# Kernel optimization log

Hardware: AMD Instinct MI355X
Metric: run time of the kernel (lower is better)

## Reference

```python
import jax, jax.numpy as jnp
import numpy as np

HIDDEN = 768
HEADS = 12
HEAD_DIM = 64
SEQ = 512
DS_K = 64  # downsampling_k
EPS = 1e-6


def setup_inputs() -> dict:
    key = jax.random.key(0)
    ks = jax.random.split(key, 16)
    B = 32
    sd = 1.0 / DS_K
    glorot = jax.nn.initializers.lecun_normal()  # flax default_kernel_init
    inp = {
        "query": jax.random.normal(ks[0], (B, SEQ, HIDDEN), jnp.float32),
        "key": jax.random.normal(ks[1], (B, SEQ, HIDDEN), jnp.float32),
        "value": jax.random.normal(ks[2], (B, SEQ, HIDDEN), jnp.float32),
        "step": 0,
        # learned Linformer-style downsampling projections [k, s]
        "W_kds": sd * jax.random.normal(ks[3], (DS_K, SEQ), jnp.float32),
        "W_vds": sd * jax.random.normal(ks[4], (DS_K, SEQ), jnp.float32),
        # DenseGeneral qkv kernels [d, n, h] and biases [n, h]
        "Wq": glorot(ks[5], (HIDDEN, HEADS, HEAD_DIM), jnp.float32),
        "bq": jnp.zeros((HEADS, HEAD_DIM), jnp.float32),
        "Wk": glorot(ks[6], (HIDDEN, HEADS, HEAD_DIM), jnp.float32),
        "bk": jnp.zeros((HEADS, HEAD_DIM), jnp.float32),
        "Wv": glorot(ks[7], (HIDDEN, HEADS, HEAD_DIM), jnp.float32),
        "bv": jnp.zeros((HEADS, HEAD_DIM), jnp.float32),
        # out projection contracts (n, h) -> hidden
        "Wout": glorot(ks[8], (HEADS * HEAD_DIM, HIDDEN), jnp.float32).reshape(HEADS, HEAD_DIM, HIDDEN),
        "bout": jnp.zeros((HIDDEN,), jnp.float32),
    }
    return inp


def reference(query, key, value, step, W_kds, W_vds, Wq, bq, Wk, bk, Wv, bv, Wout, bout):
    # Linformer-style downsample of keys/values along sequence: [b,s,d] -> [b,k,d]
    key_ds = jnp.einsum("ks,bsd->bkd", W_kds, key)
    val_ds = jnp.einsum("ks,bsd->bkd", W_vds, value)

    # per-head projections
    queries = jnp.einsum("bqd,dnh->bqnh", query, Wq) + bq    # [b,q,n,h]
    keys = jnp.einsum("bkd,dnh->bknh", key_ds, Wk) + bk      # [b,k,n,h]
    values = jnp.einsum("bkd,dnh->bknh", val_ds, Wv) + bv    # [b,k,n,h]

    # kernelized linear attention with elu feature map (mask=False path)
    phi_q = jax.nn.elu(queries) + 1.0
    phi_k = jax.nn.elu(keys) + 1.0
    s = jnp.einsum("bknd,bknh->bndh", phi_k, values)          # [b,n,h,h] KV state
    z = jnp.sum(phi_k, axis=1)                                 # [b,n,h]
    qs = jnp.einsum("bqnd,bndh->bqnh", phi_q, s)
    qz = jnp.einsum("bqnd,bnd->bqn", phi_q, z) + EPS
    a_v = qs / qz[..., None]                                   # [b,q,n,h]

    out = jnp.einsum("bqnh,nhD->bqD", a_v, Wout) + bout        # [b,q,hidden]
    return out
```

## Files before the change

kernel.cpp:

```cpp
#include <hip/hip_runtime.h>

typedef unsigned short u16;
typedef u16 u16x8 __attribute__((ext_vector_type(8)));
typedef __bf16 bf16;
typedef bf16 bf16x8 __attribute__((ext_vector_type(8)));
typedef float f32x4 __attribute__((ext_vector_type(4)));

__device__ __forceinline__ float bf2f(u16 v) {
  union { unsigned u; float f; } x; x.u = ((unsigned)v) << 16; return x.f;
}
__device__ __forceinline__ u16 f2bf(float f) {
  union { float f; unsigned u; } x; x.f = f;
  unsigned u = x.u;
  u += 0x7fffu + ((u >> 16) & 1u);
  return (u16)(u >> 16);
}

#define GLDS16(g, l) __builtin_amdgcn_global_load_lds( \
    (const __attribute__((address_space(1))) unsigned int*)(const void*)(g), \
    (__attribute__((address_space(3))) unsigned int*)(void*)(l), 16, 0, 0)

__global__ __launch_bounds__(256) void convert_k(
    const float* __restrict__ wk, const float* __restrict__ wv,
    const float* __restrict__ b0, const float* __restrict__ b1,
    const float* __restrict__ b2, const float* __restrict__ b3,
    u16* __restrict__ dstW, u16* __restrict__ dstB) {
  const int i = blockIdx.x * 256 + threadIdx.x;
  if (i < 32768)      dstW[i] = f2bf(wk[i]);
  else if (i < 65536) dstW[i] = f2bf(wv[i - 32768]);
  else {
    int j = i - 65536, s = j / 768, si = j % 768;
    const float* src = (s == 0) ? b0 : (s == 1) ? b1 : (s == 2) ? b2 : b3;
    dstB[j] = f2bf(src[si]);
  }
}

__global__ __launch_bounds__(256) void f32_to_bf16_k(
    const float* __restrict__ in, u16* __restrict__ out) {
  const int i = blockIdx.x * 256 + threadIdx.x;
  f32x4 a = *(const f32x4*)&in[(size_t)i * 8];
  f32x4 b = *(const f32x4*)&in[(size_t)i * 8 + 4];
  u16x8 w;
  #pragma unroll
  for (int j = 0; j < 4; ++j) { w[j] = f2bf(a[j]); w[4 + j] = f2bf(b[j]); }
  *(u16x8*)&out[(size_t)i * 8] = w;
}

__global__ __launch_bounds__(256) void transpose4_k(
    const float* __restrict__ w0, const float* __restrict__ w1,
    const float* __restrict__ w2, const float* __restrict__ w3,
    u16* __restrict__ out) {
  const float* W = (blockIdx.z == 0) ? w0 : (blockIdx.z == 1) ? w1 : (blockIdx.z == 2) ? w2 : w3;
  u16* O = out + (size_t)blockIdx.z * 768 * 768;
  __shared__ u16 T[64][72];
  const int t = threadIdx.x;
  const int r0 = blockIdx.x * 64, c0 = blockIdx.y * 64;
  #pragma unroll
  for (int p = 0; p < 2; ++p) {
    int v = t + p * 256;
    int r = v / 8, c = (v % 8) * 8;
    f32x4 x0 = *(const f32x4*)&W[(size_t)(r0 + r) * 768 + c0 + c];
    f32x4 x1 = *(const f32x4*)&W[(size_t)(r0 + r) * 768 + c0 + c + 4];
    #pragma unroll
    for (int i = 0; i < 4; ++i) { T[r][c + i] = f2bf(x0[i]); T[r][c + 4 + i] = f2bf(x1[i]); }
  }
  __syncthreads();
  #pragma unroll
  for (int p = 0; p < 2; ++p) {
    int v = t + p * 256;
    int r = v / 8, c = (v % 8) * 8;
    u16x8 tv;
    #pragma unroll
    for (int i = 0; i < 8; ++i) tv[i] = T[c + i][r];
    *(u16x8*)&O[(size_t)(c0 + r) * 768 + r0 + c] = tv;
  }
}

template<int ACT, bool OF32>
__global__ __launch_bounds__(256) void gemm97_k(
    const u16* __restrict__ A, int lda,
    const u16* __restrict__ Bt, int ldb,
    void* __restrict__ Craw, int ldc,
    const u16* __restrict__ bias, int K)
{
  __shared__ u16 As[128 * 32];
  __shared__ u16 Bs[128 * 32];
  const int mt = blockIdx.x * 128, nt = blockIdx.y * 128;
  const int t = threadIdx.x, wave = t >> 6, lane = t & 63;
  const int wm = (wave >> 1) * 64, wn = (wave & 1) * 64;
  const int lrow = lane & 15, quad = lane >> 4;
  f32x4 acc[4][4] = {};

  for (int k0 = 0; k0 < K; k0 += 32) {
    __syncthreads();
    #pragma unroll
    for (int p = 0; p < 2; ++p) {
      const int s = wave * 128 + p * 64 + lane;
      const int r = s >> 2, c = (s & 3) * 8;
      const int lb = (wave * 128 + p * 64) * 8;
      GLDS16(&A[(size_t)(mt + r) * lda + k0 + c], &As[lb]);
      GLDS16(&Bt[(size_t)(nt + r) * ldb + k0 + c], &Bs[lb]);
    }
    __syncthreads();

    bf16x8 av[4], bv[4];
    #pragma unroll
    for (int i = 0; i < 4; ++i) av[i] = *(const bf16x8*)&As[(wm + i * 16 + lrow) * 32 + quad * 8];
    #pragma unroll
    for (int j = 0; j < 4; ++j) bv[j] = *(const bf16x8*)&Bs[(wn + j * 16 + lrow) * 32 + quad * 8];
    #pragma unroll
    for (int i = 0; i < 4; ++i)
      #pragma unroll
      for (int j = 0; j < 4; ++j)
        acc[i][j] = __builtin_amdgcn_mfma_f32_16x16x32_bf16(av[i], bv[j], acc[i][j], 0, 0, 0);
  }

  #pragma unroll
  for (int i = 0; i < 4; ++i) {
    #pragma unroll
    for (int j = 0; j < 4; ++j) {
      const int col = nt + wn + j * 16 + lrow;
      const float badd = bias ? bf2f(bias[col]) : 0.0f;
      #pragma unroll
      for (int r = 0; r < 4; ++r) {
        const int row = mt + wm + i * 16 + quad * 4 + r;
        float v = acc[i][j][r] + badd;
        if constexpr (ACT == 1) v = v > 0.0f ? v + 1.0f : __expf(v);
        if constexpr (OF32) ((float*)Craw)[(size_t)row * ldc + col] = v;
        else                ((u16*)Craw)[(size_t)row * ldc + col] = f2bf(v);
      }
    }
  }
}

template<int BM, int BN, int BK, int WM, int WN, bool NN, int ACT,
         bool AF32, bool BF32, bool OF32>
__global__ __launch_bounds__(256) void gemm_k(
    const void* __restrict__ Araw, int lda,
    const void* __restrict__ Braw, int ldb,
    void* __restrict__ Craw, int ldc,
    const u16* __restrict__ bias,
    int K, int nDiv,
    long long offA_b, long long offA_n,
    long long offB_b, long long offB_n,
    long long offC_b, long long offC_n,
    long long offBias_b)
{
  constexpr int LDSK = BK + 8;
  __shared__ u16 As[BM][LDSK];
  __shared__ u16 Bs[BN][LDSK];

  const int z  = blockIdx.z;
  const int bb = z / nDiv, ni = z % nDiv;
  const long long dA = bb * offA_b + ni * offA_n;
  const long long dB = bb * offB_b + ni * offB_n;
  const long long dC = bb * offC_b + ni * offC_n;
  const u16*   A16 = AF32 ? nullptr : ((const u16*)Araw) + dA;
  const float* A32 = AF32 ? ((const float*)Araw) + dA : nullptr;
  const u16*   B16 = BF32 ? nullptr : ((const u16*)Braw) + dB;
  const float* B32 = BF32 ? ((const float*)Braw) + dB : nullptr;
  u16*   C16 = OF32 ? nullptr : ((u16*)Craw) + dC;
  float* C32 = OF32 ? ((float*)Craw) + dC : nullptr;
  if (bias) bias += bb * offBias_b;

  const int mt = blockIdx.x * BM;
  const int nt = blockIdx.y * BN;
  const int t = threadIdx.x;
  const int wave = t >> 6, lane = t & 63;
  constexpr int WAVES_N = BN / WN;
  const int wm = (wave / WAVES_N) * WM;
  const int wn = (wave % WAVES_N) * WN;
  constexpr int FM = WM / 16, FN = WN / 16;
  const int lrow = lane & 15, quad = lane >> 4;

  f32x4 acc[FM][FN] = {};

  for (int k0 = 0; k0 < K; k0 += BK) {
    __syncthreads();
    #pragma unroll
    for (int p = 0; p < (BM * BK / 8) / 256; ++p) {
      int v = t + p * 256;
      int r = v / (BK / 8);
      int c = (v % (BK / 8)) * 8;
      size_t idx = (size_t)(mt + r) * lda + k0 + c;
      if constexpr (!AF32) {
        *(u16x8*)&As[r][c] = *(const u16x8*)&A16[idx];
      } else {
        f32x4 x0 = *(const f32x4*)&A32[idx];
        f32x4 x1 = *(const f32x4*)&A32[idx + 4];
        u16x8 w;
        #pragma unroll
        for (int i = 0; i < 4; ++i) { w[i] = f2bf(x0[i]); w[4 + i] = f2bf(x1[i]); }
        *(u16x8*)&As[r][c] = w;
      }
    }
    if constexpr (!NN) {
      #pragma unroll
      for (int p = 0; p < (BN * BK / 8) / 256; ++p) {
        int v = t + p * 256;
        int r = v / (BK / 8);
        int c = (v % (BK / 8)) * 8;
        size_t idx = (size_t)(nt + r) * ldb + k0 + c;
        if constexpr (!BF32) {
          *(u16x8*)&Bs[r][c] = *(const u16x8*)&B16[idx];
        } else {
          f32x4 x0 = *(const f32x4*)&B32[idx];
          f32x4 x1 = *(const f32x4*)&B32[idx + 4];
          u16x8 w;
          #pragma unroll
          for (int i = 0; i < 4; ++i) { w[i] = f2bf(x0[i]); w[4 + i] = f2bf(x1[i]); }
          *(u16x8*)&Bs[r][c] = w;
        }
      }
    } else {
      static_assert(!NN || (BN == 128 && BK == 32), "NN staging is fixed-shape");
      int n  = t & 127;
      int kh = (t >> 7) * 16;
      u16x8 t0, t1;
      if constexpr (!BF32) {
        #pragma unroll
        for (int i = 0; i < 8; ++i) t0[i] = B16[(size_t)(k0 + kh + i) * ldb + nt + n];
        #pragma unroll
        for (int i = 0; i < 8; ++i) t1[i] = B16[(size_t)(k0 + kh + 8 + i) * ldb + nt + n];
      } else {
        #pragma unroll
        for (int i = 0; i < 8; ++i) t0[i] = f2bf(B32[(size_t)(k0 + kh + i) * ldb + nt + n]);
        #pragma unroll
        for (int i = 0; i < 8; ++i) t1[i] = f2bf(B32[(size_t)(k0 + kh + 8 + i) * ldb + nt + n]);
      }
      *(u16x8*)&Bs[n][kh]     = t0;
      *(u16x8*)&Bs[n][kh + 8] = t1;
    }
    __syncthreads();

    bf16x8 av[FM], bv[FN];
    #pragma unroll
    for (int i = 0; i < FM; ++i) av[i] = *(const bf16x8*)&As[wm + i * 16 + lrow][quad * 8];
    #pragma unroll
    for (int j = 0; j < FN; ++j) bv[j] = *(const bf16x8*)&Bs[wn + j * 16 + lrow][quad * 8];
    #pragma unroll
    for (int i = 0; i < FM; ++i)
      #pragma unroll
      for (int j = 0; j < FN; ++j)
        acc[i][j] = __builtin_amdgcn_mfma_f32_16x16x32_bf16(av[i], bv[j], acc[i][j], 0, 0, 0);
  }

  #pragma unroll
  for (int i = 0; i < FM; ++i) {
    #pragma unroll
    for (int j = 0; j < FN; ++j) {
      const int col = nt + wn + j * 16 + lrow;
      float badd = bias ? bf2f(bias[col]) : 0.0f;
      #pragma unroll
      for (int r = 0; r < 4; ++r) {
        const int row = mt + wm + i * 16 + quad * 4 + r;
        float v = acc[i][j][r] + badd;
        if constexpr (ACT == 1) v = v > 0.0f ? v + 1.0f : __expf(v);
        if constexpr (ACT == 3) { if (bb == 0) v = v > 0.0f ? v + 1.0f : __expf(v); }
        if constexpr (OF32) C32[(size_t)row * ldc + col] = v;
        else                C16[(size_t)row * ldc + col] = f2bf(v);
      }
    }
  }
}

__global__ __launch_bounds__(256) void kv_state_k(
    const u16* __restrict__ phi_k, const u16* __restrict__ vals,
    u16* __restrict__ sT, float* __restrict__ z)
{
  __shared__ float pk[64][65];
  __shared__ float vv[64][65];
  const int x = blockIdx.x;
  const int b = x / 12, n = x % 12;
  const int t = threadIdx.x;
  const u16* pkg = phi_k + (size_t)b * 64 * 768 + n * 64;
  const u16* vvg = vals  + (size_t)b * 64 * 768 + n * 64;
  #pragma unroll
  for (int p = 0; p < 2; ++p) {
    int v = t + p * 256;
    int r = v / 8, c = (v % 8) * 8;
    u16x8 a  = *(const u16x8*)&pkg[(size_t)r * 768 + c];
    u16x8 bq = *(const u16x8*)&vvg[(size_t)r * 768 + c];
    #pragma unroll
    for (int i = 0; i < 8; ++i) { pk[r][c + i] = bf2f(a[i]); vv[r][c + i] = bf2f(bq[i]); }
  }
  __syncthreads();
  const int d0 = (t >> 4) * 4, h0 = (t & 15) * 4;
  float s4[4][4] = {};
  for (int k = 0; k < 64; ++k) {
    float pv[4], vb[4];
    #pragma unroll
    for (int i = 0; i < 4; ++i) { pv[i] = pk[k][d0 + i]; vb[i] = vv[k][h0 + i]; }
    #pragma unroll
    for (int i = 0; i < 4; ++i)
      #pragma unroll
      for (int j = 0; j < 4; ++j) s4[i][j] += pv[i] * vb[j];
  }
  const size_t base = (size_t)x * 4096;
  #pragma unroll
  for (int i = 0; i < 4; ++i)
    #pragma unroll
    for (int j = 0; j < 4; ++j)
      sT[base + (size_t)(h0 + j) * 64 + d0 + i] = f2bf(s4[i][j]);
  if (t < 64) {
    float zz = 0.f;
    for (int k = 0; k < 64; ++k) zz += pk[k][t];
    z[(size_t)x * 64 + t] = zz;
  }
}

__global__ __launch_bounds__(256) void attn_av_k(
    u16* __restrict__ phi_q,
    const u16* __restrict__ sT,
    const float* __restrict__ zbuf)
{
  __shared__ u16 As[64 * 72];
  __shared__ u16 Bs[64 * 72];
  __shared__ float zv[64];
  __shared__ float zpart[4][64];
  __shared__ float zq[64];
  const int x = blockIdx.x, y = blockIdx.y;
  const int b = y / 12, n = y % 12;
  const int t = threadIdx.x;
  u16* Abase = phi_q + (size_t)b * 512 * 768 + (size_t)x * 64 * 768 + n * 64;
  const u16* Bbase = sT + (size_t)y * 4096;
  if (t < 64) zv[t] = zbuf[(size_t)y * 64 + t];
  #pragma unroll
  for (int p = 0; p < 2; ++p) {
    int v = t + p * 256;
    int r = v >> 3, c = (v & 7) * 8;
    *(u16x8*)&As[r * 72 + c] = *(const u16x8*)&Abase[(size_t)r * 768 + c];
    *(u16x8*)&Bs[r * 72 + c] = *(const u16x8*)&Bbase[r * 64 + c];
  }
  __syncthreads();
  {
    int r = t & 63, seg = t >> 6;
    float s = 0.f;
    #pragma unroll
    for (int j = 0; j < 16; ++j) s += bf2f(As[r * 72 + seg * 16 + j]) * zv[seg * 16 + j];
    zpart[seg][r] = s;
  }
  __syncthreads();
  if (t < 64) {
    float s = zpart[0][t] + zpart[1][t] + zpart[2][t] + zpart[3][t];
    zq[t] = 1.0f / (s + 1e-6f);
  }
  const int wave = t >> 6, lane = t & 63;
  const int wm = (wave >> 1) * 32, wn = (wave & 1) * 32;
  const int lrow = lane & 15, quad = lane >> 4;
  f32x4 acc[2][2] = {};
  #pragma unroll
  for (int c = 0; c < 2; ++c) {
    bf16x8 av[2], bv[2];
    #pragma unroll
    for (int i = 0; i < 2; ++i) av[i] = *(const bf16x8*)&As[(wm + i * 16 + lrow) * 72 + c * 32 + quad * 8];
    #pragma unroll
    for (int j = 0; j < 2; ++j) bv[j] = *(const bf16x8*)&Bs[(wn + j * 16 + lrow) * 72 + c * 32 + quad * 8];
    #pragma unroll
    for (int i = 0; i < 2; ++i)
      #pragma unroll
      for (int j = 0; j < 2; ++j)
        acc[i][j] = __builtin_amdgcn_mfma_f32_16x16x32_bf16(av[i], bv[j], acc[i][j], 0, 0, 0);
  }
  __syncthreads();
  #pragma unroll
  for (int i = 0; i < 2; ++i)
    #pragma unroll
    for (int j = 0; j < 2; ++j) {
      const int col = wn + j * 16 + lrow;
      #pragma unroll
      for (int r = 0; r < 4; ++r) {
        const int row = wm + i * 16 + quad * 4 + r;
        Abase[(size_t)row * 768 + col] = f2bf(acc[i][j][r] * zq[row]);
      }
    }
}

__global__ void tagfill_k(float* out, float val, int n) {
  int i = blockIdx.x * 256 + threadIdx.x;
  if (i < n) out[i] = val;
}

extern "C" void kernel_launch(void* const* d_in, const int* in_sizes, int n_in,
                              void* d_out, int out_size, void* d_ws, size_t ws_size,
                              hipStream_t stream) {
  (void)out_size;
  float* out = (float*)d_out;

  int o;
  if (n_in >= 14 && in_sizes[3] == 1) o = 4;
  else if (n_in == 13) o = 3;
  else { tagfill_k<<<4, 256, 0, stream>>>(out, 77.0f, 1024); return; }
  if (in_sizes[0] != 12582912 || in_sizes[o + 0] != 32768 || in_sizes[o + 2] != 589824) {
    tagfill_k<<<4, 256, 0, stream>>>(out, 88.0f, 1024); return;
  }

  const float* query = (const float*)d_in[0];
  const float* key   = (const float*)d_in[1];
  const float* value = (const float*)d_in[2];
  const float* W_kds = (const float*)d_in[o + 0];
  const float* W_vds = (const float*)d_in[o + 1];
  const float* Wq   = (const float*)d_in[o + 2];
  const float* bq   = (const float*)d_in[o + 3];
  const float* Wk   = (const float*)d_in[o + 4];
  const float* bk   = (const float*)d_in[o + 5];
  const float* Wv   = (const float*)d_in[o + 6];
  const float* bv   = (const float*)d_in[o + 7];
  const float* Wout = (const float*)d_in[o + 8];
  const float* bout = (const float*)d_in[o + 9];

  const size_t NEED_SMALL = 42604544;
  const size_t NEED_BIG   = 55187456;
  if (ws_size < NEED_SMALL) { tagfill_k<<<4, 256, 0, stream>>>(out, 123.0f, 1024); return; }
  const bool big = (ws_size >= NEED_BIG);

  char* base = (char*)d_ws;
  u16 *WT, *q_bf = nullptr, *key_ds, *val_ds, *phi_k, *vals, *phi_q, *sT, *Wds_c, *bias_c;
  float* zbuf;
  WT = (u16*)base;
  if (big) {
    char* B = base + 4718592;
    q_bf   = (u16*)B;
    key_ds = (u16*)B;
    val_ds = (u16*)(B + 3145728);
    phi_k  = (u16*)(B + 6291456);
    vals   = (u16*)(B + 9437184);
    sT     = (u16*)B;
    zbuf   = (float*)(B + 3145728);
    phi_q  = (u16*)(base + 29884416);
    Wds_c  = (u16*)(base + 55050240);
    bias_c = (u16*)(base + 55181312);
  } else {
    key_ds = (u16*)(base + 4718592);
    val_ds = (u16*)(base + 7864320);
    sT     = (u16*)(base + 4718592);
    zbuf   = (float*)(base + 7864320);
    phi_k  = (u16*)(base + 11010048);
    vals   = (u16*)(base + 14155776);
    phi_q  = (u16*)(base + 17301504);
    Wds_c  = (u16*)(base + 42467328);
    bias_c = (u16*)(base + 42598400);
  }
  u16* a_v = phi_q;
  u16* WqT   = WT;
  u16* WkT   = WT + 768 * 768;
  u16* WvT   = WT + 2 * 768 * 768;
  u16* WoutT = WT + 3 * 768 * 768;
  u16* Wkds_c = Wds_c;
  u16* Wvds_c = Wds_c + 32768;
  u16* bq_c = bias_c, *bk_c = bias_c + 768, *bv_c = bias_c + 1536, *bout_c = bias_c + 2304;

  convert_k<<<268, 256, 0, stream>>>(W_kds, W_vds, bq, bk, bv, bout, Wds_c, bias_c);
  transpose4_k<<<dim3(12, 12, 4), 256, 0, stream>>>(Wq, Wk, Wv, Wout, WT);

  if (big) {
    f32_to_bf16_k<<<6144, 256, 0, stream>>>(query, q_bf);
    gemm97_k<1, false><<<dim3(128, 6), 256, 0, stream>>>(
        q_bf, 768, WqT, 768, phi_q, 768, bq_c, 768);
  } else {
    gemm_k<128, 128, 32, 64, 64, false, 1, true, false, false><<<dim3(128, 6, 1), 256, 0, stream>>>(
        query, 768, WqT, 768, phi_q, 768, bq_c, 768, 1, 0, 0, 0, 0, 0, 0, 0);
  }

  gemm_k<64, 128, 32, 64, 32, true, 0, false, true, false><<<dim3(1, 6, 32), 256, 0, stream>>>(
      Wkds_c, 512, key, 768, key_ds, 768, nullptr, 512, 1,
      0, 0, (long long)512 * 768, 0, (long long)64 * 768, 0, 0);
  gemm_k<64, 128, 32, 64, 32, true, 0, false, true, false><<<dim3(1, 6, 32), 256, 0, stream>>>(
      Wvds_c, 512, value, 768, val_ds, 768, nullptr, 512, 1,
      0, 0, (long long)512 * 768, 0, (long long)64 * 768, 0, 0);

  gemm_k<64, 64, 32, 32, 32, false, 3, false, false, false><<<dim3(32, 12, 2), 256, 0, stream>>>(
      key_ds, 768, WkT, 768, phi_k, 768, bk_c, 768, 1,
      1572864, 0, 589824, 0, 1572864, 0, 768);

  kv_state_k<<<dim3(384), 256, 0, stream>>>(phi_k, vals, sT, zbuf);

  attn_av_k<<<dim3(8, 384), 256, 0, stream>>>(phi_q, sT, zbuf);

  gemm97_k<0, true><<<dim3(128, 6), 256, 0, stream>>>(
      a_v, 768, WoutT, 768, out, 768, bout_c, 768);
}
```

Measured before the change: 329.1 us.

## Merge prep kernels into one launch and fuse key/value downsampling GEMMs

Three preprocessing kernels (weight transpose, query bf16 conversion, small weight/bias conversion) are merged into one launch with block-range dispatch. The two separate key/value downsampling GEMMs become a single ds_k kernel covering both, with coalesced row-wise f32 loads that are converted and transposed into shared memory. The small-workspace fallback path is removed and the generic GEMM template is specialised. This cuts launch count and improves the strided B loads of the old NN staging, but the downsampling kernel runs only 384 blocks with a 64-row tile.

Measured after the change: 313.3 us. 1.05x faster.

```diff
diff --git a/kernel.cpp b/kernel.cpp
--- a/kernel.cpp
+++ b/kernel.cpp
@@ -20,60 +20,117 @@
     (const __attribute__((address_space(1))) unsigned int*)(const void*)(g), \
     (__attribute__((address_space(3))) unsigned int*)(void*)(l), 16, 0, 0)
 
-__global__ __launch_bounds__(256) void convert_k(
-    const float* __restrict__ wk, const float* __restrict__ wv,
+__global__ __launch_bounds__(256) void prep_k(
+    const float* __restrict__ Wq, const float* __restrict__ Wk,
+    const float* __restrict__ Wv, const float* __restrict__ Wout,
+    const float* __restrict__ query,
+    const float* __restrict__ wkds, const float* __restrict__ wvds,
     const float* __restrict__ b0, const float* __restrict__ b1,
     const float* __restrict__ b2, const float* __restrict__ b3,
-    u16* __restrict__ dstW, u16* __restrict__ dstB) {
-  const int i = blockIdx.x * 256 + threadIdx.x;
-  if (i < 32768)      dstW[i] = f2bf(wk[i]);
-  else if (i < 65536) dstW[i] = f2bf(wv[i - 32768]);
-  else {
-    int j = i - 65536, s = j / 768, si = j % 768;
-    const float* src = (s == 0) ? b0 : (s == 1) ? b1 : (s == 2) ? b2 : b3;
-    dstB[j] = f2bf(src[si]);
-  }
-}
-
-__global__ __launch_bounds__(256) void f32_to_bf16_k(
-    const float* __restrict__ in, u16* __restrict__ out) {
-  const int i = blockIdx.x * 256 + threadIdx.x;
-  f32x4 a = *(const f32x4*)&in[(size_t)i * 8];
-  f32x4 b = *(const f32x4*)&in[(size_t)i * 8 + 4];
-  u16x8 w;
-  #pragma unroll
-  for (int j = 0; j < 4; ++j) { w[j] = f2bf(a[j]); w[4 + j] = f2bf(b[j]); }
-  *(u16x8*)&out[(size_t)i * 8] = w;
-}
-
-__global__ __launch_bounds__(256) void transpose4_k(
-    const float* __restrict__ w0, const float* __restrict__ w1,
-    const float* __restrict__ w2, const float* __restrict__ w3,
-    u16* __restrict__ out) {
-  const float* W = (blockIdx.z == 0) ? w0 : (blockIdx.z == 1) ? w1 : (blockIdx.z == 2) ? w2 : w3;
-  u16* O = out + (size_t)blockIdx.z * 768 * 768;
+    u16* __restrict__ WT, u16* __restrict__ q_bf,
+    u16* __restrict__ dstW, u16* __restrict__ dstB)
+{
   __shared__ u16 T[64][72];
+  const int blk = blockIdx.x;
   const int t = threadIdx.x;
-  const int r0 = blockIdx.x * 64, c0 = blockIdx.y * 64;
-  #pragma unroll
-  for (int p = 0; p < 2; ++p) {
-    int v = t + p * 256;
-    int r = v / 8, c = (v % 8) * 8;
-    f32x4 x0 = *(const f32x4*)&W[(size_t)(r0 + r) * 768 + c0 + c];
-    f32x4 x1 = *(const f32x4*)&W[(size_t)(r0 + r) * 768 + c0 + c + 4];
-    #pragma unroll
-    for (int i = 0; i < 4; ++i) { T[r][c + i] = f2bf(x0[i]); T[r][c + 4 + i] = f2bf(x1[i]); }
-  }
-  __syncthreads();
-  #pragma unroll
-  for (int p = 0; p < 2; ++p) {
-    int v = t + p * 256;
-    int r = v / 8, c = (v % 8) * 8;
-    u16x8 tv;
-    #pragma unroll
-    for (int i = 0; i < 8; ++i) tv[i] = T[c + i][r];
-    *(u16x8*)&O[(size_t)(c0 + r) * 768 + r0 + c] = tv;
-  }
+  if (blk < 576) {
+    const int bz = blk / 144, rr = blk % 144;
+    const int r0 = (rr / 12) * 64, c0 = (rr % 12) * 64;
+    const float* W = (bz == 0) ? Wq : (bz == 1) ? Wk : (bz == 2) ? Wv : Wout;
+    u16* O = WT + (size_t)bz * 768 * 768;
+    #pragma unroll
+    for (int p = 0; p < 2; ++p) {
+      int v = t + p * 256;
+      int r = v / 8, c = (v % 8) * 8;
+      f32x4 x0 = *(const f32x4*)&W[(size_t)(r0 + r) * 768 + c0 + c];
+      f32x4 x1 = *(const f32x4*)&W[(size_t)(r0 + r) * 768 + c0 + c + 4];
+      #pragma unroll
+      for (int i = 0; i < 4; ++i) { T[r][c + i] = f2bf(x0[i]); T[r][c + 4 + i] = f2bf(x1[i]); }
+    }
+    __syncthreads();
+    #pragma unroll
+    for (int p = 0; p < 2; ++p) {
+      int v = t + p * 256;
+      int r = v / 8, c = (v % 8) * 8;
+      u16x8 tv;
+      #pragma unroll
+      for (int i = 0; i < 8; ++i) tv[i] = T[c + i][r];
+      *(u16x8*)&O[(size_t)(c0 + r) * 768 + r0 + c] = tv;
+    }
+  } else if (blk < 6720) {
+    const size_t i = (size_t)(blk - 576) * 256 + t;
+    f32x4 a = *(const f32x4*)&query[i * 8];
+    f32x4 b = *(const f32x4*)&query[i * 8 + 4];
+    u16x8 w;
+    #pragma unroll
+    for (int j = 0; j < 4; ++j) { w[j] = f2bf(a[j]); w[4 + j] = f2bf(b[j]); }
+    *(u16x8*)&q_bf[i * 8] = w;
+  } else {
+    const int i = (blk - 6720) * 256 + t;
+    if (i < 32768)      dstW[i] = f2bf(wkds[i]);
+    else if (i < 65536) dstW[i] = f2bf(wvds[i - 32768]);
+    else {
+      int j = i - 65536, s = j / 768, si = j % 768;
+      const float* src = (s == 0) ? b0 : (s == 1) ? b1 : (s == 2) ? b2 : b3;
+      dstB[j] = f2bf(src[si]);
+    }
+  }
+}
+
+__global__ __launch_bounds__(256) void ds_k(
+    const u16* __restrict__ Wds,
+    const float* __restrict__ key, const float* __restrict__ value,
+    u16* __restrict__ key_ds)
+{
+  __shared__ u16 As[64][40];
+  __shared__ u16 Bs[128][36];
+  const int pair = blockIdx.y >> 5, b = blockIdx.y & 31;
+  const float* src = (pair ? value : key) + (size_t)b * 512 * 768;
+  const u16* W = Wds + pair * 32768;
+  u16* dst = key_ds + (size_t)pair * 1572864 + (size_t)b * 49152;
+  const int nt = blockIdx.x * 128;
+  const int t = threadIdx.x, wave = t >> 6, lane = t & 63;
+  const int wm = (wave >> 1) * 32, wn = (wave & 1) * 64;
+  const int lrow = lane & 15, quad = lane >> 4;
+  const int kk = t >> 5, n4 = (t & 31) * 4;
+
+  f32x4 acc[2][4] = {};
+  for (int k0 = 0; k0 < 512; k0 += 32) {
+    __syncthreads();
+    {
+      int r = t >> 2, c = (t & 3) * 8;
+      *(u16x8*)&As[r][c] = *(const u16x8*)&W[(size_t)r * 512 + k0 + c];
+    }
+    #pragma unroll
+    for (int p = 0; p < 4; ++p) {
+      int k = kk + p * 8;
+      f32x4 x = *(const f32x4*)&src[(size_t)(k0 + k) * 768 + nt + n4];
+      #pragma unroll
+      for (int i = 0; i < 4; ++i) Bs[n4 + i][k] = f2bf(x[i]);
+    }
+    __syncthreads();
+    bf16x8 av[2], bv[4];
+    #pragma unroll
+    for (int i = 0; i < 2; ++i) av[i] = *(const bf16x8*)&As[wm + i * 16 + lrow][quad * 8];
+    #pragma unroll
+    for (int j = 0; j < 4; ++j) bv[j] = *(const bf16x8*)&Bs[wn + j * 16 + lrow][quad * 8];
+    #pragma unroll
+    for (int i = 0; i < 2; ++i)
+      #pragma unroll
+      for (int j = 0; j < 4; ++j)
+        acc[i][j] = __builtin_amdgcn_mfma_f32_16x16x32_bf16(av[i], bv[j], acc[i][j], 0, 0, 0);
+  }
+  #pragma unroll
+  for (int i = 0; i < 2; ++i)
+    #pragma unroll
+    for (int j = 0; j < 4; ++j) {
+      const int col = nt + wn + j * 16 + lrow;
+      #pragma unroll
+      for (int r = 0; r < 4; ++r) {
+        const int row = wm + i * 16 + quad * 4 + r;
+        dst[(size_t)row * 768 + col] = f2bf(acc[i][j][r]);
+      }
+    }
 }
 
 template<int ACT, bool OF32>
@@ -133,36 +190,20 @@
   }
 }
 
-template<int BM, int BN, int BK, int WM, int WN, bool NN, int ACT,
-         bool AF32, bool BF32, bool OF32>
-__global__ __launch_bounds__(256) void gemm_k(
-    const void* __restrict__ Araw, int lda,
-    const void* __restrict__ Braw, int ldb,
-    void* __restrict__ Craw, int ldc,
+template<int BM, int BN, int BK, int WM, int WN>
+__global__ __launch_bounds__(256) void gemmkv_k(
+    const u16* __restrict__ A, int lda,
+    const u16* __restrict__ B, int ldb,
+    u16* __restrict__ C, int ldc,
     const u16* __restrict__ bias,
-    int K, int nDiv,
-    long long offA_b, long long offA_n,
-    long long offB_b, long long offB_n,
-    long long offC_b, long long offC_n,
-    long long offBias_b)
+    int K,
+    long long offA_b, long long offB_b, long long offC_b, long long offBias_b)
 {
   constexpr int LDSK = BK + 8;
   __shared__ u16 As[BM][LDSK];
   __shared__ u16 Bs[BN][LDSK];
-
-  const int z  = blockIdx.z;
-  const int bb = z / nDiv, ni = z % nDiv;
-  const long long dA = bb * offA_b + ni * offA_n;
-  const long long dB = bb * offB_b + ni * offB_n;
-  const long long dC = bb * offC_b + ni * offC_n;
-  const u16*   A16 = AF32 ? nullptr : ((const u16*)Araw) + dA;
-  const float* A32 = AF32 ? ((const float*)Araw) + dA : nullptr;
-  const u16*   B16 = BF32 ? nullptr : ((const u16*)Braw) + dB;
-  const float* B32 = BF32 ? ((const float*)Braw) + dB : nullptr;
-  u16*   C16 = OF32 ? nullptr : ((u16*)Craw) + dC;
-  float* C32 = OF32 ? ((float*)Craw) + dC : nullptr;
-  if (bias) bias += bb * offBias_b;
-
+  const int bb = blockIdx.z;
+  A += bb * offA_b; B += bb * offB_b; C += bb * offC_b; bias += bb * offBias_b;
   const int mt = blockIdx.x * BM;
   const int nt = blockIdx.y * BN;
   const int t = threadIdx.x;
@@ -172,7 +213,6 @@
   const int wn = (wave % WAVES_N) * WN;
   constexpr int FM = WM / 16, FN = WN / 16;
   const int lrow = lane & 15, quad = lane >> 4;
-
   f32x4 acc[FM][FN] = {};
 
   for (int k0 = 0; k0 < K; k0 += BK) {
@@ -180,59 +220,16 @@
     #pragma unroll
     for (int p = 0; p < (BM * BK / 8) / 256; ++p) {
       int v = t + p * 256;
-      int r = v / (BK / 8);
-      int c = (v % (BK / 8)) * 8;
-      size_t idx = (size_t)(mt + r) * lda + k0 + c;
-      if constexpr (!AF32) {
-        *(u16x8*)&As[r][c] = *(const u16x8*)&A16[idx];
-      } else {
-        f32x4 x0 = *(const f32x4*)&A32[idx];
-        f32x4 x1 = *(const f32x4*)&A32[idx + 4];
-        u16x8 w;
-        #pragma unroll
-        for (int i = 0; i < 4; ++i) { w[i] = f2bf(x0[i]); w[4 + i] = f2bf(x1[i]); }
-        *(u16x8*)&As[r][c] = w;
-      }
-    }
-    if constexpr (!NN) {
-      #pragma unroll
-      for (int p = 0; p < (BN * BK / 8) / 256; ++p) {
-        int v = t + p * 256;
-        int r = v / (BK / 8);
-        int c = (v % (BK / 8)) * 8;
-        size_t idx = (size_t)(nt + r) * ldb + k0 + c;
-        if constexpr (!BF32) {
-          *(u16x8*)&Bs[r][c] = *(const u16x8*)&B16[idx];
-        } else {
-          f32x4 x0 = *(const f32x4*)&B32[idx];
-          f32x4 x1 = *(const f32x4*)&B32[idx + 4];
-          u16x8 w;
-          #pragma unroll
-          for (int i = 0; i < 4; ++i) { w[i] = f2bf(x0[i]); w[4 + i] = f2bf(x1[i]); }
-          *(u16x8*)&Bs[r][c] = w;
-        }
-      }
-    } else {
-      static_assert(!NN || (BN == 128 && BK == 32), "NN staging is fixed-shape");
-      int n  = t & 127;
-      int kh = (t >> 7) * 16;
-      u16x8 t0, t1;
-      if constexpr (!BF32) {
-        #pragma unroll
-        for (int i = 0; i < 8; ++i) t0[i] = B16[(size_t)(k0 + kh + i) * ldb + nt + n];
-        #pragma unroll
-        for (int i = 0; i < 8; ++i) t1[i] = B16[(size_t)(k0 + kh + 8 + i) * ldb + nt + n];
-      } else {
-        #pragma unroll
-        for (int i = 0; i < 8; ++i) t0[i] = f2bf(B32[(size_t)(k0 + kh + i) * ldb + nt + n]);
-        #pragma unroll
-        for (int i = 0; i < 8; ++i) t1[i] = f2bf(B32[(size_t)(k0 + kh + 8 + i) * ldb + nt + n]);
-      }
-      *(u16x8*)&Bs[n][kh]     = t0;
-      *(u16x8*)&Bs[n][kh + 8] = t1;
-    }
-    __syncthreads();
-
+      int r = v / (BK / 8), c = (v % (BK / 8)) * 8;
+      *(u16x8*)&As[r][c] = *(const u16x8*)&A[(size_t)(mt + r) * lda + k0 + c];
+    }
+    #pragma unroll
+    for (int p = 0; p < (BN * BK / 8) / 256; ++p) {
+      int v = t + p * 256;
+      int r = v / (BK / 8), c = (v % (BK / 8)) * 8;
+      *(u16x8*)&Bs[r][c] = *(const u16x8*)&B[(size_t)(nt + r) * ldb + k0 + c];
+    }
+    __syncthreads();
     bf16x8 av[FM], bv[FN];
     #pragma unroll
     for (int i = 0; i < FM; ++i) av[i] = *(const bf16x8*)&As[wm + i * 16 + lrow][quad * 8];
@@ -244,24 +241,20 @@
       for (int j = 0; j < FN; ++j)
         acc[i][j] = __builtin_amdgcn_mfma_f32_16x16x32_bf16(av[i], bv[j], acc[i][j], 0, 0, 0);
   }
-
-  #pragma unroll
-  for (int i = 0; i < FM; ++i) {
+  #pragma unroll
+  for (int i = 0; i < FM; ++i)
     #pragma unroll
     for (int j = 0; j < FN; ++j) {
       const int col = nt + wn + j * 16 + lrow;
-      float badd = bias ? bf2f(bias[col]) : 0.0f;
+      const float badd = bf2f(bias[col]);
       #pragma unroll
       for (int r = 0; r < 4; ++r) {
         const int row = mt + wm + i * 16 + quad * 4 + r;
         float v = acc[i][j][r] + badd;
-        if constexpr (ACT == 1) v = v > 0.0f ? v + 1.0f : __expf(v);
-        if constexpr (ACT == 3) { if (bb == 0) v = v > 0.0f ? v + 1.0f : __expf(v); }
-        if constexpr (OF32) C32[(size_t)row * ldc + col] = v;
-        else                C16[(size_t)row * ldc + col] = f2bf(v);
+        if (bb == 0) v = v > 0.0f ? v + 1.0f : __expf(v);
+        C[(size_t)row * ldc + col] = f2bf(v);
       }
     }
-  }
 }
 
 __global__ __launch_bounds__(256) void kv_state_k(
@@ -310,9 +303,7 @@
 }
 
 __global__ __launch_bounds__(256) void attn_av_k(
-    u16* __restrict__ phi_q,
-    const u16* __restrict__ sT,
-    const float* __restrict__ zbuf)
+    u16* __restrict__ phi_q, const u16* __restrict__ sT, const float* __restrict__ zbuf)
 {
   __shared__ u16 As[64 * 72];
   __shared__ u16 Bs[64 * 72];
@@ -409,69 +400,38 @@
   const float* Wout = (const float*)d_in[o + 8];
   const float* bout = (const float*)d_in[o + 9];
 
-  const size_t NEED_SMALL = 42604544;
-  const size_t NEED_BIG   = 55187456;
-  if (ws_size < NEED_SMALL) { tagfill_k<<<4, 256, 0, stream>>>(out, 123.0f, 1024); return; }
-  const bool big = (ws_size >= NEED_BIG);
+  const size_t NEED = 55187456;
+  if (ws_size < NEED) { tagfill_k<<<4, 256, 0, stream>>>(out, 123.0f, 1024); return; }
 
   char* base = (char*)d_ws;
-  u16 *WT, *q_bf = nullptr, *key_ds, *val_ds, *phi_k, *vals, *phi_q, *sT, *Wds_c, *bias_c;
-  float* zbuf;
-  WT = (u16*)base;
-  if (big) {
-    char* B = base + 4718592;
-    q_bf   = (u16*)B;
-    key_ds = (u16*)B;
-    val_ds = (u16*)(B + 3145728);
-    phi_k  = (u16*)(B + 6291456);
-    vals   = (u16*)(B + 9437184);
-    sT     = (u16*)B;
-    zbuf   = (float*)(B + 3145728);
-    phi_q  = (u16*)(base + 29884416);
-    Wds_c  = (u16*)(base + 55050240);
-    bias_c = (u16*)(base + 55181312);
-  } else {
-    key_ds = (u16*)(base + 4718592);
-    val_ds = (u16*)(base + 7864320);
-    sT     = (u16*)(base + 4718592);
-    zbuf   = (float*)(base + 7864320);
-    phi_k  = (u16*)(base + 11010048);
-    vals   = (u16*)(base + 14155776);
-    phi_q  = (u16*)(base + 17301504);
-    Wds_c  = (u16*)(base + 42467328);
-    bias_c = (u16*)(base + 42598400);
-  }
+  u16*   WT     = (u16*)base;
+  char*  Breg   = base + 4718592;
+  u16*   q_bf   = (u16*)Breg;
+  u16*   key_ds = (u16*)Breg;
+  u16*   sT     = (u16*)Breg;
+  float* zbuf   = (float*)(Breg + 3145728);
+  u16*   phi_k  = (u16*)(Breg + 6291456);
+  u16*   vals   = (u16*)(Breg + 9437184);
+  u16*   phi_q  = (u16*)(base + 29884416);
+  u16*   Wds_c  = (u16*)(base + 55050240);
+  u16*   bias_c = (u16*)(base + 55181312);
   u16* a_v = phi_q;
   u16* WqT   = WT;
   u16* WkT   = WT + 768 * 768;
-  u16* WvT   = WT + 2 * 768 * 768;
   u16* WoutT = WT + 3 * 768 * 768;
-  u16* Wkds_c = Wds_c;
-  u16* Wvds_c = Wds_c + 32768;
-  u16* bq_c = bias_c, *bk_c = bias_c + 768, *bv_c = bias_c + 1536, *bout_c = bias_c + 2304;
-
-  convert_k<<<268, 256, 0, stream>>>(W_kds, W_vds, bq, bk, bv, bout, Wds_c, bias_c);
-  transpose4_k<<<dim3(12, 12, 4), 256, 0, stream>>>(Wq, Wk, Wv, Wout, WT);
-
-  if (big) {
-    f32_to_bf16_k<<<6144, 256, 0, stream>>>(query, q_bf);
-    gemm97_k<1, false><<<dim3(128, 6), 256, 0, stream>>>(
-        q_bf, 768, WqT, 768, phi_q, 768, bq_c, 768);
-  } else {
-    gemm_k<128, 128, 32, 64, 64, false, 1, true, false, false><<<dim3(128, 6, 1), 256, 0, stream>>>(
-        query, 768, WqT, 768, phi_q, 768, bq_c, 768, 1, 0, 0, 0, 0, 0, 0, 0);
-  }
-
-  gemm_k<64, 128, 32, 64, 32, true, 0, false, true, false><<<dim3(1, 6, 32), 256, 0, stream>>>(
-      Wkds_c, 512, key, 768, key_ds, 768, nullptr, 512, 1,
-      0, 0, (long long)512 * 768, 0, (long long)64 * 768, 0, 0);
-  gemm_k<64, 128, 32, 64, 32, true, 0, false, true, false><<<dim3(1, 6, 32), 256, 0, stream>>>(
-      Wvds_c, 512, value, 768, val_ds, 768, nullptr, 512, 1,
-      0, 0, (long long)512 * 768, 0, (long long)64 * 768, 0, 0);
-
-  gemm_k<64, 64, 32, 32, 32, false, 3, false, false, false><<<dim3(32, 12, 2), 256, 0, stream>>>(
-      key_ds, 768, WkT, 768, phi_k, 768, bk_c, 768, 1,
-      1572864, 0, 589824, 0, 1572864, 0, 768);
+  u16* bq_c = bias_c, *bk_c = bias_c + 768, *bout_c = bias_c + 2304;
+
+  prep_k<<<6988, 256, 0, stream>>>(Wq, Wk, Wv, Wout, query, W_kds, W_vds,
+                                   bq, bk, bv, bout, WT, q_bf, Wds_c, bias_c);
+
+  gemm97_k<1, false><<<dim3(128, 6), 256, 0, stream>>>(
+      q_bf, 768, WqT, 768, phi_q, 768, bq_c, 768);
+
+  ds_k<<<dim3(6, 64), 256, 0, stream>>>(Wds_c, key, value, key_ds);
+
+  gemmkv_k<64, 64, 32, 32, 32><<<dim3(32, 12, 2), 256, 0, stream>>>(
+      key_ds, 768, WkT, 768, phi_k, 768, bk_c, 768,
+      1572864, 589824, 1572864, 768);
 
   kv_state_k<<<dim3(384), 256, 0, stream>>>(phi_k, vals, sT, zbuf);
 
```
